# Performance work log

Hardware: AMD Instinct MI355X
Metric: run time of the kernel (lower is better)

The kernel has to match this reference:

```python
import jax, jax.numpy as jnp
import numpy as np

H, N2, R = 512, 16, 32   # hidden_dim, state_dim//2, dt_rank=ceil(512/16)
B, L = 1, 4096


def setup_inputs() -> dict:
    key = jax.random.key(0)
    ks = jax.random.split(key, 7)
    u = jax.random.normal(ks[0], (B, L, H), dtype=jnp.float32)
    # Parameter initialization mirroring S4DKernel.__init__
    A_log = jnp.zeros((H, N2), jnp.float32)                      # log(ones)
    A_im = jnp.broadcast_to(jnp.arange(N2, dtype=jnp.float32), (H, N2)).copy()
    B_param = jax.random.normal(ks[1], (H, N2, 2), jnp.float32)
    C_param = jax.random.normal(ks[2], (H, N2, 2), jnp.float32)
    D = jax.random.normal(ks[3], (H,), jnp.float32)
    dt_w = jax.random.normal(ks[4], (H, R), jnp.float32) / np.sqrt(R)
    dt_min, dt_max, dt_floor = 1e-3, 0.1, 1e-4
    dt_init = jnp.exp(jax.random.uniform(ks[5], (H,), jnp.float32)
                      * (np.log(dt_max) - np.log(dt_floor)) + np.log(dt_floor))
    dt_init = jnp.maximum(dt_init, dt_min)
    dt_b = dt_init + jnp.log(-jnp.expm1(-dt_init))               # inverse-softplus init
    xproj_w = jax.random.normal(ks[6], (R, H), jnp.float32) / np.sqrt(H)
    return {"u": u, "A_log": A_log, "A_im": A_im, "B_param": B_param,
            "C_param": C_param, "D": D, "dt_w": dt_w, "dt_b": dt_b,
            "xproj_w": xproj_w}


def reference(u, A_log, A_im, B_param, C_param, D, dt_w, dt_b, xproj_w):
    # Complex continuous-time parameters
    A = -jnp.exp(A_log) + 1j * A_im                 # [H, N2]
    Bc = B_param[..., 0] + 1j * B_param[..., 1]     # [H, N2]
    Cc = C_param[..., 0] + 1j * C_param[..., 1]     # [H, N2]

    # dt path: x_proj_for_dt (no bias) -> dt_proj -> softplus
    dt_u = jnp.einsum('blh,rh->blr', u, xproj_w)                    # [B,L,R]
    dt = jax.nn.softplus(jnp.einsum('blr,hr->blh', dt_u, dt_w) + dt_b)  # [B,L,H]

    # ZOH discretization
    z = dt[..., None] * A                           # [B,L,H,N2] complex
    A_bar = jnp.exp(z)
    B_bar_div = jnp.where(jnp.abs(z) < 1e-4, 1.0 + z / 2, (jnp.exp(z) - 1.0) / z)
    ub = u[..., None].astype(A_bar.dtype) * B_bar_div * Bc          # [B,L,H,N2]

    # Parallel scan for h_k = A_k * h_{k-1} + u_k (first-order linear recurrence)
    def op(c1, c2):
        a1, b1 = c1
        a2, b2 = c2
        return a1 * a2, a2 * b1 + b2
    _, h = jax.lax.associative_scan(op, (A_bar, ub), axis=1)        # [B,L,H,N2]

    y = jnp.einsum('blhn,hn->blh', h, Cc) + u * D
    return y.real
```

## Files before the change

### kernel.cpp

```cpp
#include <hip/hip_runtime.h>

#define Hd 512
#define N2d 16
#define Rd 32
#define Ld 4096
#define NCHUNK 128
#define CLEN (Ld / NCHUNK)
#define NCH (Hd * N2d)
#define NGRP 16
#define NGROUPS (NCHUNK / NGRP)

__global__ __launch_bounds__(256) void k_dt(const float* __restrict__ u,
                                            const float* __restrict__ xproj_w,
                                            const float* __restrict__ dt_w,
                                            const float* __restrict__ dt_b,
                                            float2* __restrict__ du_out) {
    __shared__ float u_s[8][Hd];
    __shared__ float dtu_s[8][Rd];
    const int t = threadIdx.x;
    const int l0 = blockIdx.x * 8;

    #pragma unroll
    for (int i = 0; i < 16; ++i) {
        int idx = t + i * 256;
        ((float*)u_s)[idx] = u[l0 * Hd + idx];
    }
    __syncthreads();

    const int r = t >> 3;
    const int j = t & 7;
    float part[8];
    #pragma unroll
    for (int l = 0; l < 8; ++l) part[l] = 0.f;
    for (int k = 0; k < 64; ++k) {
        float w = xproj_w[r * Hd + k * 8 + j];
        #pragma unroll
        for (int l = 0; l < 8; ++l) part[l] = fmaf(u_s[l][k * 8 + j], w, part[l]);
    }
    #pragma unroll
    for (int off = 1; off < 8; off <<= 1) {
        #pragma unroll
        for (int l = 0; l < 8; ++l) part[l] += __shfl_xor(part[l], off);
    }
    if (j == 0) {
        #pragma unroll
        for (int l = 0; l < 8; ++l) dtu_s[l][r] = part[l];
    }
    __syncthreads();

    #pragma unroll
    for (int hb = 0; hb < 2; ++hb) {
        int h = hb * 256 + t;
        float bias = dt_b[h];
        float acc[8];
        #pragma unroll
        for (int l = 0; l < 8; ++l) acc[l] = bias;
        #pragma unroll
        for (int rb = 0; rb < 8; ++rb) {
            float4 w = *(const float4*)&dt_w[h * Rd + rb * 4];
            #pragma unroll
            for (int l = 0; l < 8; ++l) {
                acc[l] = fmaf(dtu_s[l][rb * 4 + 0], w.x, acc[l]);
                acc[l] = fmaf(dtu_s[l][rb * 4 + 1], w.y, acc[l]);
                acc[l] = fmaf(dtu_s[l][rb * 4 + 2], w.z, acc[l]);
                acc[l] = fmaf(dtu_s[l][rb * 4 + 3], w.w, acc[l]);
            }
        }
        #pragma unroll
        for (int l = 0; l < 8; ++l) {
            float x = acc[l];
            float sp = fmaxf(x, 0.f) + log1pf(__expf(-fabsf(x)));
            float uv = u_s[l][h];
            float us = uv * __builtin_amdgcn_rcpf(fmaxf(sp, 1e-30f));
            du_out[(l0 + l) * Hd + h] = make_float2(sp, us);
        }
    }
}

__global__ __launch_bounds__(256) void k_chunk(const float2* __restrict__ du,
        const float* __restrict__ A_log, const float* __restrict__ A_im,
        const float* __restrict__ B_param, const float* __restrict__ C_param,
        const float* __restrict__ Dp,
        float2* __restrict__ Sb, float* __restrict__ Tc,
        float2* __restrict__ y1T) {
    const int t = threadIdx.x;
    const int q = t & 3;
    const int hh = blockIdx.y * 64 + (t >> 2);
    const int c = blockIdx.x;
    const int hnb = hh * N2d + q * 4;
    const int lbase = c * CLEN;

    float alog[4], Aim[4];
    #pragma unroll
    for (int j = 0; j < 4; ++j) {
        alog[j] = A_log[hnb + j];
        Aim[j] = A_im[hnb + j];
    }
    float d1 = Aim[1] - Aim[0], d2 = Aim[2] - Aim[1], d3 = Aim[3] - Aim[2];
    const bool fast = (alog[1] == alog[0]) && (alog[2] == alog[0]) &&
                      (alog[3] == alog[0]) && (d1 == d2) && (d2 == d3);
    float Are[4];
    if (fast) {
        Are[0] = -__expf(alog[0]);
        Are[1] = Are[2] = Are[3] = Are[0];
    } else {
        #pragma unroll
        for (int j = 0; j < 4; ++j) Are[j] = -__expf(alog[j]);
    }
    float BAr[4], BAi[4], Cre[4], Cim[4];
    #pragma unroll
    for (int j = 0; j < 4; ++j) {
        int hn = hnb + j;
        float Bre = B_param[2 * hn];
        float Bim = B_param[2 * hn + 1];
        float inv = __builtin_amdgcn_rcpf(Are[j] * Are[j] + Aim[j] * Aim[j]);
        BAr[j] = (Bre * Are[j] + Bim * Aim[j]) * inv;
        BAi[j] = (Bim * Are[j] - Bre * Aim[j]) * inv;
        Cre[j] = C_param[2 * hn];
        Cim[j] = C_param[2 * hn + 1];
    }
    const float Dv = Dp[hh];

    float sr[4] = {0.f, 0.f, 0.f, 0.f}, si[4] = {0.f, 0.f, 0.f, 0.f};
    float sdt = 0.f;

    float2 b0[8], b1[8];

    #define LOADB(buf, bb)                                                     \
        { _Pragma("unroll")                                                    \
          for (int k = 0; k < 8; ++k)                                          \
              buf[k] = du[(lbase + (bb) * 8 + k) * Hd + hh]; }

    if (fast) {
        const float Are0 = Are[0], Aim0 = Aim[0], dA = Aim[1] - Aim[0];
        #define STEPF(buf, bb)                                                 \
            { _Pragma("unroll")                                                \
              for (int k = 0; k < 8; ++k) {                                    \
                int l = lbase + (bb) * 8 + k;                                  \
                float dtv = buf[k].x, us = buf[k].y;                           \
                sdt += dtv;                                                    \
                float er = __expf(dtv * Are0);                                 \
                float s0, c0, sd, cd;                                          \
                __sincosf(dtv * Aim0, &s0, &c0);                               \
                __sincosf(dtv * dA, &sd, &cd);                                 \
                float ar = er * c0, ai = er * s0;                              \
                float yv = 0.f;                                                \
                _Pragma("unroll")                                              \
                for (int jj = 0; jj < 4; ++jj) {                               \
                    float gr = fmaf(ar, us, -us);                              \
                    float gi = ai * us;                                        \
                    float nr = fmaf(ar, sr[jj], fmaf(-ai, si[jj],              \
                                 fmaf(gr, BAr[jj], -gi * BAi[jj])));           \
                    float ni = fmaf(ar, si[jj], fmaf( ai, sr[jj],              \
                                 fmaf(gr, BAi[jj],  gi * BAr[jj])));           \
                    sr[jj] = nr; si[jj] = ni;                                  \
                    yv = fmaf(nr, Cre[jj], fmaf(-ni, Cim[jj], yv));            \
                    if (jj < 3) {                                              \
                        float tr = fmaf(ar, cd, -ai * sd);                     \
                        ai = fmaf(ai, cd, ar * sd);                            \
                        ar = tr;                                               \
                    }                                                          \
                }                                                              \
                yv += __shfl_xor(yv, 1);                                       \
                yv += __shfl_xor(yv, 2);                                       \
                if (q == 0)                                                    \
                    y1T[l * Hd + hh] = make_float2(fmaf(dtv * us, Dv, yv), sdt);\
              } }
        LOADB(b0, 0);
        LOADB(b1, 1); STEPF(b0, 0);
        LOADB(b0, 2); STEPF(b1, 1);
        LOADB(b1, 3); STEPF(b0, 2);
        STEPF(b1, 3);
        #undef STEPF
    } else {
        #define STEPS(buf, bb)                                                 \
            { _Pragma("unroll")                                                \
              for (int k = 0; k < 8; ++k) {                                    \
                int l = lbase + (bb) * 8 + k;                                  \
                float dtv = buf[k].x, us = buf[k].y;                           \
                sdt += dtv;                                                    \
                float yv = 0.f;                                                \
                _Pragma("unroll")                                              \
                for (int jj = 0; jj < 4; ++jj) {                               \
                    float er = __expf(dtv * Are[jj]);                          \
                    float s, cc;                                               \
                    __sincosf(dtv * Aim[jj], &s, &cc);                         \
                    float ar = er * cc, ai = er * s;                           \
                    float gr = fmaf(ar, us, -us);                              \
                    float gi = ai * us;                                        \
                    float nr = fmaf(ar, sr[jj], fmaf(-ai, si[jj],              \
                                 fmaf(gr, BAr[jj], -gi * BAi[jj])));           \
                    float ni = fmaf(ar, si[jj], fmaf( ai, sr[jj],              \
                                 fmaf(gr, BAi[jj],  gi * BAr[jj])));           \
                    sr[jj] = nr; si[jj] = ni;                                  \
                    yv = fmaf(nr, Cre[jj], fmaf(-ni, Cim[jj], yv));            \
                }                                                              \
                yv += __shfl_xor(yv, 1);                                       \
                yv += __shfl_xor(yv, 2);                                       \
                if (q == 0)                                                    \
                    y1T[l * Hd + hh] = make_float2(fmaf(dtv * us, Dv, yv), sdt);\
              } }
        LOADB(b0, 0);
        LOADB(b1, 1); STEPS(b0, 0);
        LOADB(b0, 2); STEPS(b1, 1);
        LOADB(b1, 3); STEPS(b0, 2);
        STEPS(b1, 3);
        #undef STEPS
    }
    #undef LOADB

    int base = c * NCH + hnb;
    #pragma unroll
    for (int jj = 0; jj < 4; ++jj)
        Sb[base + jj] = make_float2(sr[jj], si[jj]);
    if (q == 0) Tc[hh * NCHUNK + c] = sdt;
}

__global__ __launch_bounds__(256) void k_comb(const float2* __restrict__ Sb,
        const float* __restrict__ Tc, const float* __restrict__ A_log,
        const float* __restrict__ A_im, const float* __restrict__ C_param,
        float2* __restrict__ W) {
    __shared__ float4 agg_s[32][NGROUPS + 1];
    __shared__ float Tc_s[2][NCHUNK];
    const int t = threadIdx.x;
    const int g = t >> 5;
    const int cl = t & 31;
    const int chain = blockIdx.x * 32 + cl;
    const int h0 = blockIdx.x * 2;

    {
        int cc = t & 127;
        int hs = t >> 7;
        Tc_s[hs][cc] = Tc[(h0 + hs) * NCHUNK + cc];
    }
    __syncthreads();

    const int hsel = cl >> 4;
    const float Are = -__expf(A_log[chain]);
    const float Aim = A_im[chain];

    float2 s[NGRP];
    float pr[NGRP], pi[NGRP];
    #pragma unroll
    for (int i = 0; i < NGRP; ++i) {
        int c = g * NGRP + i;
        s[i] = Sb[c * NCH + chain];
        float T = Tc_s[hsel][c];
        float er = __expf(Are * T);
        float sn, cs;
        __sincosf(Aim * T, &sn, &cs);
        pr[i] = er * cs;
        pi[i] = er * sn;
    }

    float Pr = 1.f, Pi = 0.f, Hr = 0.f, Hi = 0.f;
    #pragma unroll
    for (int i = 0; i < NGRP; ++i) {
        float nhr = fmaf(pr[i], Hr, fmaf(-pi[i], Hi, s[i].x));
        float nhi = fmaf(pr[i], Hi, fmaf( pi[i], Hr, s[i].y));
        float npr = fmaf(pr[i], Pr, -pi[i] * Pi);
        float npi = fmaf(pr[i], Pi,  pi[i] * Pr);
        Hr = nhr; Hi = nhi; Pr = npr; Pi = npi;
    }
    agg_s[cl][g] = make_float4(Pr, Pi, Hr, Hi);
    __syncthreads();

    float hr = 0.f, hi = 0.f;
    for (int j = 0; j < g; ++j) {
        float4 a = agg_s[cl][j];
        float nr = fmaf(a.x, hr, fmaf(-a.y, hi, a.z));
        float ni = fmaf(a.x, hi, fmaf( a.y, hr, a.w));
        hr = nr; hi = ni;
    }

    const float Cr = C_param[2 * chain];
    const float Ci = C_param[2 * chain + 1];
    #pragma unroll
    for (int i = 0; i < NGRP; ++i) {
        int c = g * NGRP + i;
        W[c * NCH + chain] = make_float2(fmaf(Cr, hr, -Ci * hi),
                                         fmaf(Cr, hi,  Ci * hr));
        float nr = fmaf(pr[i], hr, fmaf(-pi[i], hi, s[i].x));
        float ni = fmaf(pr[i], hi, fmaf( pi[i], hr, s[i].y));
        hr = nr; hi = ni;
    }
}

__global__ __launch_bounds__(256) void k_corr(const float2* __restrict__ y1T,
        const float* __restrict__ A_log, const float* __restrict__ A_im,
        const float2* __restrict__ W, float* __restrict__ out) {
    const int t = threadIdx.x;
    const int c = blockIdx.x;
    const int hl = t & 63;
    const int h = blockIdx.y * 64 + hl;
    const int lb = t >> 6;
    const int l0 = c * CLEN + lb * 8;
    const int hn0 = h * N2d;

    float2 yt[8];
    #pragma unroll
    for (int k = 0; k < 8; ++k) yt[k] = y1T[(l0 + k) * Hd + h];

    float2 w[N2d];
    {
        const float4* w4 = reinterpret_cast<const float4*>(&W[c * NCH + hn0]);
        #pragma unroll
        for (int n = 0; n < 8; ++n) {
            float4 v = w4[n];
            w[2 * n]     = make_float2(v.x, v.y);
            w[2 * n + 1] = make_float2(v.z, v.w);
        }
    }

    float alog[N2d], aim[N2d];
    #pragma unroll
    for (int n = 0; n < N2d; ++n) {
        alog[n] = A_log[hn0 + n];
        aim[n] = A_im[hn0 + n];
    }
    float dA = aim[1] - aim[0];
    bool fast = true;
    #pragma unroll
    for (int n = 1; n < N2d; ++n)
        fast = fast && (alog[n] == alog[0]) && (aim[n] - aim[n - 1] == dA);

    if (fast) {
        const float Are0 = -__expf(alog[0]);
        const float Aim0 = aim[0];
        #pragma unroll
        for (int k = 0; k < 8; ++k) {
            float T = yt[k].y;
            float er = __expf(Are0 * T);
            float s0, c0, sd, cd;
            __sincosf(Aim0 * T, &s0, &c0);
            __sincosf(dA * T, &sd, &cd);
            float ar = er * c0, ai = er * s0;
            float corr = 0.f;
            #pragma unroll
            for (int n = 0; n < N2d; ++n) {
                corr = fmaf(ar, w[n].x, fmaf(-ai, w[n].y, corr));
                if (n < N2d - 1) {
                    float tr = fmaf(ar, cd, -ai * sd);
                    ai = fmaf(ai, cd, ar * sd);
                    ar = tr;
                }
            }
            out[(l0 + k) * Hd + h] = yt[k].x + corr;
        }
    } else {
        float are[N2d];
        #pragma unroll
        for (int n = 0; n < N2d; ++n) are[n] = -__expf(alog[n]);
        #pragma unroll
        for (int k = 0; k < 8; ++k) {
            float T = yt[k].y;
            float corr = 0.f;
            #pragma unroll
            for (int n = 0; n < N2d; ++n) {
                float er = __expf(are[n] * T);
                float s, cc;
                __sincosf(aim[n] * T, &s, &cc);
                corr = fmaf(er * cc, w[n].x, fmaf(-er * s, w[n].y, corr));
            }
            out[(l0 + k) * Hd + h] = yt[k].x + corr;
        }
    }
}

extern "C" void kernel_launch(void* const* d_in, const int* in_sizes, int n_in,
                              void* d_out, int out_size, void* d_ws, size_t ws_size,
                              hipStream_t stream) {
    const float* u        = (const float*)d_in[0];
    const float* A_log    = (const float*)d_in[1];
    const float* A_im     = (const float*)d_in[2];
    const float* B_param  = (const float*)d_in[3];
    const float* C_param  = (const float*)d_in[4];
    const float* Dp       = (const float*)d_in[5];
    const float* dt_w     = (const float*)d_in[6];
    const float* dt_b     = (const float*)d_in[7];
    const float* xproj_w  = (const float*)d_in[8];

    float2* du  = (float2*)d_ws;
    float2* Sb  = du + (size_t)Ld * Hd;
    float2* W   = Sb + (size_t)NCHUNK * NCH;
    float2* y1T = W + (size_t)NCHUNK * NCH;
    float*  Tc  = (float*)(y1T + (size_t)Ld * Hd);
    float*  out = (float*)d_out;

    k_dt<<<Ld / 8, 256, 0, stream>>>(u, xproj_w, dt_w, dt_b, du);
    dim3 g2(NCHUNK, Hd / 64);
    k_chunk<<<g2, 256, 0, stream>>>(du, A_log, A_im, B_param, C_param, Dp,
                                    Sb, Tc, y1T);
    k_comb<<<NCH / 32, 256, 0, stream>>>(Sb, Tc, A_log, A_im, C_param, W);
    k_corr<<<g2, 256, 0, stream>>>(y1T, A_log, A_im, W, out);
}
```

Measured before the change: 132.1 us.

## Store du and y1T intermediates in chunk-major per-channel layout with float4 accesses

Changes the layout of the du and y1T intermediate buffers from [L][H] to [chunk][H][CLEN], so each channel's 32 timesteps within a chunk are contiguous. Producers and consumers now read and write float4 vectors along time instead of making strided per-timestep float2 accesses. The idea is to cut the number of memory transactions in the scan kernels. In exchange, adjacent threads now hit addresses CLEN*8 bytes apart, which reduces coalescing across lanes, and y1T writes are buffered in registers before a vectorized store.

```diff
diff --git a/kernel.cpp b/kernel.cpp
--- a/kernel.cpp
+++ b/kernel.cpp
@@ -10,6 +10,7 @@
 #define NGRP 16
 #define NGROUPS (NCHUNK / NGRP)
 
+
 __global__ __launch_bounds__(256) void k_dt(const float* __restrict__ u,
                                             const float* __restrict__ xproj_w,
                                             const float* __restrict__ dt_w,
@@ -19,6 +20,8 @@
     __shared__ float dtu_s[8][Rd];
     const int t = threadIdx.x;
     const int l0 = blockIdx.x * 8;
+    const int cch = l0 >> 5;
+    const int lp  = l0 & 31;
 
     #pragma unroll
     for (int i = 0; i < 16; ++i) {
@@ -66,14 +69,20 @@
                 acc[l] = fmaf(dtu_s[l][rb * 4 + 3], w.w, acc[l]);
             }
         }
+        float2 vals[8];
         #pragma unroll
         for (int l = 0; l < 8; ++l) {
             float x = acc[l];
             float sp = fmaxf(x, 0.f) + log1pf(__expf(-fabsf(x)));
             float uv = u_s[l][h];
             float us = uv * __builtin_amdgcn_rcpf(fmaxf(sp, 1e-30f));
-            du_out[(l0 + l) * Hd + h] = make_float2(sp, us);
-        }
+            vals[l] = make_float2(sp, us);
+        }
+        float4* d4 = (float4*)&du_out[((size_t)cch * Hd + h) * CLEN + lp];
+        #pragma unroll
+        for (int i = 0; i < 4; ++i)
+            d4[i] = make_float4(vals[2 * i].x, vals[2 * i].y,
+                                vals[2 * i + 1].x, vals[2 * i + 1].y);
     }
 }
 
@@ -88,7 +97,9 @@
     const int hh = blockIdx.y * 64 + (t >> 2);
     const int c = blockIdx.x;
     const int hnb = hh * N2d + q * 4;
-    const int lbase = c * CLEN;
+
+    const float2* rowb = du + ((size_t)c * Hd + hh) * CLEN;
+    float2* y1row = y1T + ((size_t)c * Hd + hh) * CLEN;
 
     float alog[4], Aim[4];
     #pragma unroll
@@ -127,16 +138,29 @@
     float2 b0[8], b1[8];
 
     #define LOADB(buf, bb)                                                     \
-        { _Pragma("unroll")                                                    \
-          for (int k = 0; k < 8; ++k)                                          \
-              buf[k] = du[(lbase + (bb) * 8 + k) * Hd + hh]; }
+        { const float4* r4 = (const float4*)(rowb + (bb) * 8);                 \
+          _Pragma("unroll")                                                    \
+          for (int k4 = 0; k4 < 4; ++k4) {                                     \
+              float4 v = r4[k4];                                               \
+              buf[2 * k4]     = make_float2(v.x, v.y);                         \
+              buf[2 * k4 + 1] = make_float2(v.z, v.w);                         \
+          } }
+
+    #define YWRITE(bb)                                                         \
+        if (q == 0) {                                                          \
+            float4* y4 = (float4*)(y1row + (bb) * 8);                          \
+            _Pragma("unroll")                                                  \
+            for (int i = 0; i < 4; ++i)                                        \
+                y4[i] = make_float4(yb[2 * i].x, yb[2 * i].y,                  \
+                                    yb[2 * i + 1].x, yb[2 * i + 1].y);         \
+        }
 
     if (fast) {
         const float Are0 = Are[0], Aim0 = Aim[0], dA = Aim[1] - Aim[0];
         #define STEPF(buf, bb)                                                 \
-            { _Pragma("unroll")                                                \
+            { float2 yb[8];                                                    \
+              _Pragma("unroll")                                                \
               for (int k = 0; k < 8; ++k) {                                    \
-                int l = lbase + (bb) * 8 + k;                                  \
                 float dtv = buf[k].x, us = buf[k].y;                           \
                 sdt += dtv;                                                    \
                 float er = __expf(dtv * Are0);                                 \
@@ -163,9 +187,9 @@
                 }                                                              \
                 yv += __shfl_xor(yv, 1);                                       \
                 yv += __shfl_xor(yv, 2);                                       \
-                if (q == 0)                                                    \
-                    y1T[l * Hd + hh] = make_float2(fmaf(dtv * us, Dv, yv), sdt);\
-              } }
+                yb[k] = make_float2(fmaf(dtv * us, Dv, yv), sdt);              \
+              }                                                                \
+              YWRITE(bb) }
         LOADB(b0, 0);
         LOADB(b1, 1); STEPF(b0, 0);
         LOADB(b0, 2); STEPF(b1, 1);
@@ -174,9 +198,9 @@
         #undef STEPF
     } else {
         #define STEPS(buf, bb)                                                 \
-            { _Pragma("unroll")                                                \
+            { float2 yb[8];                                                    \
+              _Pragma("unroll")                                                \
               for (int k = 0; k < 8; ++k) {                                    \
-                int l = lbase + (bb) * 8 + k;                                  \
                 float dtv = buf[k].x, us = buf[k].y;                           \
                 sdt += dtv;                                                    \
                 float yv = 0.f;                                                \
@@ -197,9 +221,9 @@
                 }                                                              \
                 yv += __shfl_xor(yv, 1);                                       \
                 yv += __shfl_xor(yv, 2);                                       \
-                if (q == 0)                                                    \
-                    y1T[l * Hd + hh] = make_float2(fmaf(dtv * us, Dv, yv), sdt);\
-              } }
+                yb[k] = make_float2(fmaf(dtv * us, Dv, yv), sdt);              \
+              }                                                                \
+              YWRITE(bb) }
         LOADB(b0, 0);
         LOADB(b1, 1); STEPS(b0, 0);
         LOADB(b0, 2); STEPS(b1, 1);
@@ -208,6 +232,7 @@
         #undef STEPS
     }
     #undef LOADB
+    #undef YWRITE
 
     int base = c * NCH + hnb;
     #pragma unroll
@@ -298,8 +323,15 @@
     const int hn0 = h * N2d;
 
     float2 yt[8];
-    #pragma unroll
-    for (int k = 0; k < 8; ++k) yt[k] = y1T[(l0 + k) * Hd + h];
+    {
+        const float4* y4 = (const float4*)(y1T + ((size_t)c * Hd + h) * CLEN + lb * 8);
+        #pragma unroll
+        for (int i = 0; i < 4; ++i) {
+            float4 v = y4[i];
+            yt[2 * i]     = make_float2(v.x, v.y);
+            yt[2 * i + 1] = make_float2(v.z, v.w);
+        }
+    }
 
     float2 w[N2d];
     {
```

After: 132.4 us. No clear change (+0.2%).
